# Performance work log

Measured on AMD Instinct MI355X. Metric: run time of the kernel, lower is better.

The kernel has to match this reference:

```python
import jax, jax.numpy as jnp
import numpy as np

C = 32          # d_model / channels
D_STATE = 32
D_CONV = 4
EXPAND = 2
D_INNER = EXPAND * C          # 64
DT_RANK = (C + 15) // 16      # ceil(32/16) = 2
EPS = 1e-5


def _conv2d(x, w, b):
    # x: (B,C,H,W), w: (O,I,3,3), stride 1, padding 1 (torch Conv2d)
    y = jax.lax.conv_general_dilated(
        x, w, window_strides=(1, 1), padding=[(1, 1), (1, 1)],
        dimension_numbers=("NCHW", "OIHW", "NCHW"))
    return y + b[None, :, None, None]


def _silu(x):
    return x * jax.nn.sigmoid(x)


def _mamba(xs, in_proj_w, conv1d_w, conv1d_b, x_proj_w, dt_proj_w, dt_proj_b,
           A_log, Dp, out_proj_w):
    # xs: (B, L, C)
    xz = xs @ in_proj_w.T                       # (B, L, 2*D_INNER)
    xm, z = jnp.split(xz, 2, axis=-1)           # each (B, L, D_INNER)

    # causal depthwise conv1d along L (torch: padding=d_conv-1 then [..., :L])
    xc = xm.transpose(0, 2, 1)                  # (B, D_INNER, L)
    xc = jax.lax.conv_general_dilated(
        xc, conv1d_w, window_strides=(1,), padding=[(D_CONV - 1, 0)],
        dimension_numbers=("NCH", "OIH", "NCH"),
        feature_group_count=D_INNER)
    xm = _silu((xc + conv1d_b[None, :, None]).transpose(0, 2, 1))  # (B,L,D_INNER)

    x_dbl = xm @ x_proj_w.T                     # (B, L, DT_RANK + 2*D_STATE)
    dt = x_dbl[..., :DT_RANK]
    Bm = x_dbl[..., DT_RANK:DT_RANK + D_STATE]  # (B, L, N)
    Cm = x_dbl[..., DT_RANK + D_STATE:]         # (B, L, N)

    delta = jax.nn.softplus(dt @ dt_proj_w.T + dt_proj_b)  # (B, L, D_INNER)
    A = -jnp.exp(A_log)                                     # (D_INNER, N)

    deltaA = jnp.exp(delta[..., None] * A)                           # (B,L,D,N)
    deltaBx = delta[..., None] * Bm[:, :, None, :] * xm[..., None]   # (B,L,D,N)

    def combine(c1, c2):
        a1, b1 = c1
        a2, b2 = c2
        return a1 * a2, a2 * b1 + b2

    # parallel linear recurrence h_t = deltaA_t * h_{t-1} + deltaBx_t
    _, hstate = jax.lax.associative_scan(combine, (deltaA, deltaBx), axis=1)

    y = jnp.einsum("bldn,bln->bld", hstate, Cm) + xm * Dp
    y = y * _silu(z)
    return y @ out_proj_w.T                     # (B, L, C)


def setup_inputs() -> dict:
    key = jax.random.key(0)
    ks = jax.random.split(key, 16)
    s = 0.02
    inp = {
        "x": jax.random.normal(ks[0], (4, C, 64, 64), dtype=jnp.float32),
        "conv1_w": jax.random.normal(ks[1], (2 * C, C, 3, 3), jnp.float32) * s,
        "conv1_b": jnp.zeros((2 * C,), jnp.float32),
        "conv2_w": jax.random.normal(ks[2], (C, 2 * C, 3, 3), jnp.float32) * s,
        "conv2_b": jnp.zeros((C,), jnp.float32),
        "ln_g": jnp.ones((C,), jnp.float32),
        "ln_b": jnp.zeros((C,), jnp.float32),
        "in_proj_w": jax.random.normal(ks[3], (2 * D_INNER, C), jnp.float32) * s,
        "conv1d_w": jax.random.normal(ks[4], (D_INNER, 1, D_CONV), jnp.float32) * 0.1,
        "conv1d_b": jnp.zeros((D_INNER,), jnp.float32),
        "x_proj_w": jax.random.normal(ks[5], (DT_RANK + 2 * D_STATE, D_INNER), jnp.float32) * s,
        "dt_proj_w": jax.random.normal(ks[6], (D_INNER, DT_RANK), jnp.float32) * 0.1,
        "dt_proj_b": jax.random.normal(ks[7], (D_INNER,), jnp.float32) * 0.1 - 4.0,
        "A_log": jnp.log(jnp.tile(jnp.arange(1, D_STATE + 1, dtype=jnp.float32), (D_INNER, 1))),
        "Dp": jnp.ones((D_INNER,), jnp.float32),
        "out_proj_w": jax.random.normal(ks[8], (C, D_INNER), jnp.float32) * s,
        "smooth_w": jax.random.normal(ks[9], (C, C, 3, 3), jnp.float32) * s,
        "smooth_b": jnp.zeros((C,), jnp.float32),
    }
    return inp


def reference(x, conv1_w, conv1_b, conv2_w, conv2_b, ln_g, ln_b,
              in_proj_w, conv1d_w, conv1d_b, x_proj_w, dt_proj_w, dt_proj_b,
              A_log, Dp, out_proj_w, smooth_w, smooth_b):
    b, c, h, w = x.shape
    # convb residual
    t = jax.nn.relu(_conv2d(x, conv1_w, conv1_b))
    x = _conv2d(t, conv2_w, conv2_b) + x
    # reshape (b,c,h,w) -> (b, h*w, c) row-major (faithful to torch .reshape)
    xs = x.reshape(b, -1, c)
    # LayerNorm over last dim
    mu = jnp.mean(xs, axis=-1, keepdims=True)
    var = jnp.mean(jnp.square(xs - mu), axis=-1, keepdims=True)
    xs = (xs - mu) * jax.lax.rsqrt(var + EPS) * ln_g + ln_b
    # Mamba block
    y = _mamba(xs, in_proj_w, conv1d_w, conv1d_b, x_proj_w, dt_proj_w,
               dt_proj_b, A_log, Dp, out_proj_w)
    y = y.transpose(0, 2, 1).reshape(b, c, h, w)
    return _conv2d(y, smooth_w, smooth_b)
```

## Files before the change

kernel.cpp:

```cpp
#include <hip/hip_runtime.h>
#include <math.h>

#define SEQL 4096
#define L2E 1.44269504088896340736f

#if defined(__has_builtin)
#if __has_builtin(__builtin_amdgcn_exp2f)
#define FAST_EXP2(x) __builtin_amdgcn_exp2f(x)
#endif
#endif
#ifndef FAST_EXP2
#define FAST_EXP2(x) exp2f(x)
#endif

__device__ __forceinline__ float sigmoid_f(float x){ return 1.0f/(1.0f+expf(-x)); }

template<int CI, int CO, int COG, bool RELU, bool RES>
__global__ __launch_bounds__(256) void conv3x3_k(const float* __restrict__ in,
    const float* __restrict__ wgt, const float* __restrict__ bias,
    const float* __restrict__ res, float* __restrict__ out)
{
  constexpr int CIT = CI/4;
  __shared__ float tin[4][2][6][72];
  __shared__ float red[3][4][COG][66];
  const int tid  = threadIdx.x;
  const int lane = tid & 63;
  const int ty   = tid >> 6;
  const int h0   = blockIdx.x * 4;
  const int co0  = blockIdx.y * COG;
  const int b    = blockIdx.z;

  if (lane < 24){
    int cl = lane / 12, rem = lane % 12, r = rem >> 1, side = rem & 1;
    tin[ty][cl][r][side ? 68 : 3] = 0.0f;
  }

  float acc[4][COG];
  #pragma unroll
  for (int rr=0;rr<4;++rr)
    #pragma unroll
    for (int u=0;u<COG;++u) acc[rr][u] = 0.0f;

  const int ci0 = ty*CIT;
  for (int cig = ci0; cig < ci0 + CIT; cig += 2){
    #pragma unroll
    for (int k=0;k<3;++k){
      int idx4 = lane + k*64;
      int row  = idx4 >> 4;
      int cl   = row / 6, r = row - cl*6;
      int w4   = (idx4 & 15) << 2;
      int h    = h0 - 1 + r;
      float4 v = make_float4(0.0f,0.0f,0.0f,0.0f);
      if (h >= 0 && h < 64)
        v = *(const float4*)(in + ((size_t)(b*CI+cig+cl)*64 + h)*64 + w4);
      *(float4*)&tin[ty][cl][r][4+w4] = v;
    }
    #pragma unroll
    for (int cl=0; cl<2; ++cl){
      float rv[6][3];
      #pragma unroll
      for (int r=0;r<6;++r)
        #pragma unroll
        for (int c=0;c<3;++c)
          rv[r][c] = tin[ty][cl][r][3+lane+c];
      #pragma unroll
      for (int u=0;u<COG;++u){
        const float* wp = wgt + ((size_t)(co0+u)*CI + cig + cl)*9;
        #pragma unroll
        for (int rr=0;rr<4;++rr)
          #pragma unroll
          for (int j=0;j<3;++j){
            acc[rr][u] = fmaf(rv[rr+j][0], wp[j*3+0], acc[rr][u]);
            acc[rr][u] = fmaf(rv[rr+j][1], wp[j*3+1], acc[rr][u]);
            acc[rr][u] = fmaf(rv[rr+j][2], wp[j*3+2], acc[rr][u]);
          }
      }
    }
  }
  if (ty > 0){
    #pragma unroll
    for (int rr=0;rr<4;++rr)
      #pragma unroll
      for (int u=0;u<COG;++u) red[ty-1][rr][u][lane] = acc[rr][u];
  }
  __syncthreads();
  if (ty == 0){
    #pragma unroll
    for (int rr=0;rr<4;++rr)
      #pragma unroll
      for (int u=0;u<COG;++u){
        float s = acc[rr][u] + red[0][rr][u][lane] + red[1][rr][u][lane]
                + red[2][rr][u][lane] + bias[co0+u];
        size_t ob = ((size_t)(b*CO+co0+u)*64 + h0+rr)*64 + lane;
        if constexpr (RES)  s += res[ob];
        if constexpr (RELU) s = fmaxf(s, 0.0f);
        out[ob] = s;
      }
  }
}

__global__ __launch_bounds__(512) void mamba_in_k(const float* __restrict__ x2,
    const float* __restrict__ g, const float* __restrict__ be,
    const float* __restrict__ Wip, const float* __restrict__ cw,
    const float* __restrict__ cb, const float* __restrict__ Wxp,
    const float* __restrict__ Wdt, const float* __restrict__ bdt,
    float* __restrict__ xm2, float* __restrict__ szb, float* __restrict__ dlt,
    float* __restrict__ Bm, float* __restrict__ Cm)
{
  __shared__ float xn[68][36];
  __shared__ float xm[64][68];
  __shared__ float xt[64][68];
  __shared__ float xd[64][68];
  const int tid = threadIdx.x, lane = tid & 63, ty = tid >> 6;
  const int bi = blockIdx.x >> 6;
  const int l0 = (blockIdx.x & 63) << 6;

  if (ty < 2){
    int t = ty*64 + lane;
    if (t < 67){
      int tok = l0 - 3 + t;
      if (tok >= 0){
        const float* row = x2 + (size_t)bi*131072 + (size_t)tok*32;
        float v[32];
        #pragma unroll
        for (int c=0;c<32;c+=4){
          float4 f = *(const float4*)(row + c);
          v[c]=f.x; v[c+1]=f.y; v[c+2]=f.z; v[c+3]=f.w;
        }
        float p[8];
        #pragma unroll
        for (int j2=0;j2<8;++j2) p[j2]=v[j2];
        #pragma unroll
        for (int i=8;i<32;i+=8){
          #pragma unroll
          for (int j2=0;j2<8;++j2) p[j2]+=v[i+j2];
        }
        float mu = (((p[0]+p[1])+(p[2]+p[3]))+((p[4]+p[5])+(p[6]+p[7]))) * 0.03125f;
        float q[8];
        #pragma unroll
        for (int j2=0;j2<8;++j2){ float dd=v[j2]-mu; q[j2]=dd*dd; }
        #pragma unroll
        for (int i=8;i<32;i+=8){
          #pragma unroll
          for (int j2=0;j2<8;++j2){ float dd=v[i+j2]-mu; q[j2]+=dd*dd; }
        }
        float var = (((q[0]+q[1])+(q[2]+q[3]))+((q[4]+q[5])+(q[6]+q[7]))) * 0.03125f;
        float rstd = 1.0f / sqrtf(var + 1e-5f);
        #pragma unroll
        for (int c=0;c<32;++c) xn[t][c] = (v[c]-mu)*rstd*g[c] + be[c];
      } else {
        #pragma unroll
        for (int c=0;c<32;++c) xn[t][c] = 0.0f;
      }
    }
  }
  __syncthreads();

  const int d0 = ty*8;
  {
    float xvA[32];
    #pragma unroll
    for (int c=0;c<32;c+=4){
      float4 f = *(const float4*)(&xn[lane][c]);
      xvA[c]=f.x; xvA[c+1]=f.y; xvA[c+2]=f.z; xvA[c+3]=f.w;
    }
    #pragma unroll
    for (int jj=0;jj<8;++jj){
      const float* wr = Wip + (d0+jj)*32;
      float a = 0.0f;
      #pragma unroll
      for (int c=0;c<32;++c) a = fmaf(xvA[c], wr[c], a);
      xm[d0+jj][lane] = a;
    }
  }
  if (lane < 3){
    float xvB[32];
    #pragma unroll
    for (int c=0;c<32;c+=4){
      float4 f = *(const float4*)(&xn[64+lane][c]);
      xvB[c]=f.x; xvB[c+1]=f.y; xvB[c+2]=f.z; xvB[c+3]=f.w;
    }
    #pragma unroll
    for (int jj=0;jj<8;++jj){
      const float* wr = Wip + (d0+jj)*32;
      float a = 0.0f;
      #pragma unroll
      for (int c=0;c<32;++c) a = fmaf(xvB[c], wr[c], a);
      xm[d0+jj][64+lane] = a;
    }
  }
  {
    float xvC[32];
    #pragma unroll
    for (int c=0;c<32;c+=4){
      float4 f = *(const float4*)(&xn[lane+3][c]);
      xvC[c]=f.x; xvC[c+1]=f.y; xvC[c+2]=f.z; xvC[c+3]=f.w;
    }
    #pragma unroll
    for (int jj=0;jj<8;++jj){
      const float* wr = Wip + (64+d0+jj)*32;
      float a = 0.0f;
      #pragma unroll
      for (int c=0;c<32;++c) a = fmaf(xvC[c], wr[c], a);
      szb[((size_t)(bi*64+d0+jj))*SEQL + l0 + lane] = a * sigmoid_f(a);
    }
  }
  __syncthreads();

  #pragma unroll
  for (int jj=0;jj<8;++jj){
    int d = d0 + jj;
    float a = xm[d][lane]*cw[d*4] + xm[d][lane+1]*cw[d*4+1]
            + xm[d][lane+2]*cw[d*4+2] + xm[d][lane+3]*cw[d*4+3] + cb[d];
    float s = a * sigmoid_f(a);
    xt[lane][d] = s;
    xm2[((size_t)(bi*64+d))*SEQL + l0 + lane] = s;
  }
  __syncthreads();

  float xv[64];
  #pragma unroll
  for (int c=0;c<64;c+=4){
    float4 f = *(const float4*)(&xt[lane][c]);
    xv[c]=f.x; xv[c+1]=f.y; xv[c+2]=f.z; xv[c+3]=f.w;
  }
  for (int j=ty; j<66; j+=8){
    const float* wr = Wxp + j*64;
    float a = 0.0f;
    #pragma unroll
    for (int c=0;c<64;++c) a = fmaf(xv[c], wr[c], a);
    xd[lane][j] = a;
  }
  __syncthreads();

  float dt0 = xd[lane][0], dt1 = xd[lane][1];
  #pragma unroll
  for (int k=0;k<8;++k){
    int d2 = ty*8 + k;
    float v = dt0*Wdt[d2*2] + dt1*Wdt[d2*2+1] + bdt[d2];
    float sp = fmaxf(v,0.0f) + log1pf(expf(-fabsf(v)));
    dlt[((size_t)(bi*64+d2))*SEQL + l0 + lane] = sp;
  }
  const int which = ty >> 2, gq = ty & 3;
  float* dst = which ? Cm : Bm;
  size_t base = ((size_t)bi*SEQL + l0 + lane)*32 + gq*8;
  const int s0 = 2 + which*32 + gq*8;
  float4 f0, f1;
  f0.x = xd[lane][s0+0]; f0.y = xd[lane][s0+1]; f0.z = xd[lane][s0+2]; f0.w = xd[lane][s0+3];
  f1.x = xd[lane][s0+4]; f1.y = xd[lane][s0+5]; f1.z = xd[lane][s0+6]; f1.w = xd[lane][s0+7];
  *(float4*)(dst + base)     = f0;
  *(float4*)(dst + base + 4) = f1;
}

__global__ __launch_bounds__(256) void scan_p1(const float* __restrict__ dlt,
    const float* __restrict__ xssm, const float* __restrict__ Bm,
    const float* __restrict__ A_log, float* __restrict__ cA, float* __restrict__ cH)
{
  const int tid = threadIdx.x;
  const int n = tid & 31;
  const int chunk = (blockIdx.x & 7)*8 + (tid >> 5);
  const int bd = blockIdx.x >> 3;
  const int b = bd >> 6, d = bd & 63;
  const int l0 = chunk << 6;
  const float Av2 = -expf(A_log[d*32+n]) * L2E;
  const float* del = dlt  + (size_t)bd*SEQL + l0;
  const float* xp  = xssm + (size_t)bd*SEQL + l0;
  const float* Bp  = Bm + ((size_t)b*SEQL + l0)*32 + n;
  float h = 0.0f, aP = 1.0f;
  #pragma unroll 4
  for (int i0=0;i0<64;i0+=4){
    float4 d4 = *(const float4*)(del+i0);
    float4 x4 = *(const float4*)(xp +i0);
    float b0 = Bp[(i0+0)*32], b1 = Bp[(i0+1)*32], b2 = Bp[(i0+2)*32], b3 = Bp[(i0+3)*32];
    float a0 = FAST_EXP2(d4.x*Av2); h = fmaf(a0,h, d4.x*b0*x4.x); aP *= a0;
    float a1 = FAST_EXP2(d4.y*Av2); h = fmaf(a1,h, d4.y*b1*x4.y); aP *= a1;
    float a2 = FAST_EXP2(d4.z*Av2); h = fmaf(a2,h, d4.z*b2*x4.z); aP *= a2;
    float a3 = FAST_EXP2(d4.w*Av2); h = fmaf(a3,h, d4.w*b3*x4.w); aP *= a3;
  }
  int idx = (bd*64+chunk)*32 + n;
  cA[idx] = aP; cH[idx] = h;
}

__global__ __launch_bounds__(128) void scan_comb(const float* __restrict__ cA,
    float* __restrict__ cH)
{
  const int gid = blockIdx.x*128 + threadIdx.x;
  const int n = gid & 31, bd = gid >> 5;
  const size_t base = (size_t)bd*64*32 + n;
  float hrun = 0.0f;
  #pragma unroll 8
  for (int c=0;c<64;++c){
    float ac = cA[base + c*32];
    float hc = cH[base + c*32];
    cH[base + c*32] = hrun;
    hrun = fmaf(ac, hrun, hc);
  }
}

__global__ __launch_bounds__(256) void scan_p2(const float* __restrict__ dlt,
    const float* __restrict__ xssm, const float* __restrict__ Bm,
    const float* __restrict__ Cm, const float* __restrict__ A_log,
    const float* __restrict__ Dp, const float* __restrict__ sz,
    const float* __restrict__ cH, float* __restrict__ yt)
{
  const int tid = threadIdx.x;
  const int n = tid & 31;
  const int chunk = (blockIdx.x & 7)*8 + (tid >> 5);
  const int bd = blockIdx.x >> 3;
  const int b = bd >> 6, d = bd & 63;
  const int l0 = chunk << 6;
  const float Av2 = -expf(A_log[d*32+n]) * L2E;
  const float Dv = Dp[d];
  const float* del = dlt  + (size_t)bd*SEQL + l0;
  const float* xp  = xssm + (size_t)bd*SEQL + l0;
  const float* szp = sz   + (size_t)bd*SEQL + l0;
  const float* Bp  = Bm + ((size_t)b*SEQL + l0)*32 + n;
  const float* Cp  = Cm + ((size_t)b*SEQL + l0)*32 + n;
  float* yp = yt + (size_t)bd*SEQL + l0;
  float h = cH[(bd*64+chunk)*32 + n];
  #pragma unroll 2
  for (int i0=0;i0<64;i0+=4){
    float4 d4 = *(const float4*)(del+i0);
    float4 x4 = *(const float4*)(xp +i0);
    float4 s4 = *(const float4*)(szp+i0);
    float b0 = Bp[(i0+0)*32], b1 = Bp[(i0+1)*32], b2 = Bp[(i0+2)*32], b3 = Bp[(i0+3)*32];
    float c0 = Cp[(i0+0)*32], c1 = Cp[(i0+1)*32], c2 = Cp[(i0+2)*32], c3 = Cp[(i0+3)*32];
    float a0 = FAST_EXP2(d4.x*Av2); h = fmaf(a0,h, d4.x*b0*x4.x);
    float v0 = h*c0;
    float a1 = FAST_EXP2(d4.y*Av2); h = fmaf(a1,h, d4.y*b1*x4.y);
    float v1 = h*c1;
    float a2 = FAST_EXP2(d4.z*Av2); h = fmaf(a2,h, d4.z*b2*x4.z);
    float v2 = h*c2;
    float a3 = FAST_EXP2(d4.w*Av2); h = fmaf(a3,h, d4.w*b3*x4.w);
    float v3 = h*c3;
    v0 += __shfl_xor(v0,16); v0 += __shfl_xor(v0,8); v0 += __shfl_xor(v0,4);
    v0 += __shfl_xor(v0,2);  v0 += __shfl_xor(v0,1);
    v1 += __shfl_xor(v1,16); v1 += __shfl_xor(v1,8); v1 += __shfl_xor(v1,4);
    v1 += __shfl_xor(v1,2);  v1 += __shfl_xor(v1,1);
    v2 += __shfl_xor(v2,16); v2 += __shfl_xor(v2,8); v2 += __shfl_xor(v2,4);
    v2 += __shfl_xor(v2,2);  v2 += __shfl_xor(v2,1);
    v3 += __shfl_xor(v3,16); v3 += __shfl_xor(v3,8); v3 += __shfl_xor(v3,4);
    v3 += __shfl_xor(v3,2);  v3 += __shfl_xor(v3,1);
    if (n==0){
      yp[i0+0] = fmaf(x4.x, Dv, v0) * s4.x;
      yp[i0+1] = fmaf(x4.y, Dv, v1) * s4.y;
      yp[i0+2] = fmaf(x4.z, Dv, v2) * s4.z;
      yp[i0+3] = fmaf(x4.w, Dv, v3) * s4.w;
    }
  }
}

__global__ __launch_bounds__(512) void outproj_k(const float* __restrict__ yt,
    const float* __restrict__ Wout, float* __restrict__ ym)
{
  __shared__ float ys[64][68];
  const int tid = threadIdx.x, lane = tid & 63, ty = tid >> 6;
  const int bi = blockIdx.x >> 6;
  const int l0 = (blockIdx.x & 63) << 6;
  for (int r=ty; r<64; r+=8)
    ys[lane][r] = yt[((size_t)(bi*64+r))*SEQL + l0 + lane];
  __syncthreads();
  float yv[64];
  #pragma unroll
  for (int c=0;c<64;c+=4){
    float4 f = *(const float4*)(&ys[lane][c]);
    yv[c]=f.x; yv[c+1]=f.y; yv[c+2]=f.z; yv[c+3]=f.w;
  }
  #pragma unroll
  for (int jj=0;jj<4;++jj){
    int j = ty*4 + jj;
    const float* wr = Wout + j*64;
    float acc = 0.0f;
    #pragma unroll
    for (int c=0;c<64;++c) acc = fmaf(yv[c], wr[c], acc);
    ym[((size_t)(bi*32+j))*SEQL + l0 + lane] = acc;
  }
}

extern "C" void kernel_launch(void* const* d_in, const int* in_sizes, int n_in,
                              void* d_out, int out_size, void* d_ws, size_t ws_size,
                              hipStream_t stream) {
  const float* x        = (const float*)d_in[0];
  const float* conv1_w  = (const float*)d_in[1];
  const float* conv1_b  = (const float*)d_in[2];
  const float* conv2_w  = (const float*)d_in[3];
  const float* conv2_b  = (const float*)d_in[4];
  const float* ln_g     = (const float*)d_in[5];
  const float* ln_b     = (const float*)d_in[6];
  const float* in_proj_w= (const float*)d_in[7];
  const float* conv1d_w = (const float*)d_in[8];
  const float* conv1d_b = (const float*)d_in[9];
  const float* x_proj_w = (const float*)d_in[10];
  const float* dt_proj_w= (const float*)d_in[11];
  const float* dt_proj_b= (const float*)d_in[12];
  const float* A_log    = (const float*)d_in[13];
  const float* Dp       = (const float*)d_in[14];
  const float* out_proj_w=(const float*)d_in[15];
  const float* smooth_w = (const float*)d_in[16];
  const float* smooth_b = (const float*)d_in[17];
  float* out = (float*)d_out;

  float* ws = (float*)d_ws;
  float* t      = ws;
  float* x2     = t      + 1048576;
  float* xm2    = x2     + 524288;
  float* szb    = xm2    + 1048576;
  float* dlt    = szb    + 1048576;
  float* Bmat   = dlt    + 1048576;
  float* Cmat   = Bmat   + 524288;
  float* yt     = Cmat   + 524288;
  float* ym     = yt     + 1048576;
  float* cA     = t;
  float* cH     = t + 524288;

  conv3x3_k<32,64,4,true ,false><<<dim3(16,16,4), 256, 0, stream>>>(x,  conv1_w, conv1_b, nullptr, t);
  conv3x3_k<64,32,4,false,true ><<<dim3(16,8,4), 256, 0, stream>>>(t,  conv2_w, conv2_b, x,       x2);
  mamba_in_k  <<<256, 512, 0, stream>>>(x2, ln_g, ln_b, in_proj_w, conv1d_w, conv1d_b,
                                        x_proj_w, dt_proj_w, dt_proj_b,
                                        xm2, szb, dlt, Bmat, Cmat);
  scan_p1     <<<2048, 256, 0, stream>>>(dlt, xm2, Bmat, A_log, cA, cH);
  scan_comb   <<<64,   128, 0, stream>>>(cA, cH);
  scan_p2     <<<2048, 256, 0, stream>>>(dlt, xm2, Bmat, Cmat, A_log, Dp, szb, cH, yt);
  outproj_k   <<<256, 512, 0, stream>>>(yt, out_proj_w, ym);
  conv3x3_k<32,32,4,false,false><<<dim3(16,8,4), 256, 0, stream>>>(ym, smooth_w, smooth_b, nullptr, out);
}
```

Measured before the change: 223.6 us.

## Pad shared tiles to odd strides and transpose chunk-state layout for vectorized scan

Shared-memory row strides in the Mamba input and out-projection kernels change from multiples of 4 to odd values (37, 67). Reads switch from float4 vector loads to scalar loads, which trades fewer LDS instructions for fewer bank conflicts. The chunk carry arrays cA/cH are re-laid out so each (bd,n) pair's 64 chunks are contiguous. This lets the inter-chunk combine kernel use float4 loads and stores instead of strided scalar accesses, at the cost of strided writes in the chunk-summary kernel and strided reads in scan_p2. The conv edits are cosmetic.

```diff
diff --git a/kernel.cpp b/kernel.cpp
--- a/kernel.cpp
+++ b/kernel.cpp
@@ -45,13 +45,13 @@
   for (int cig = ci0; cig < ci0 + CIT; cig += 2){
     #pragma unroll
     for (int k=0;k<3;++k){
-      int idx4 = lane + k*64;
+      int idx4 = lane + (k<<6);
       int row  = idx4 >> 4;
-      int cl   = row / 6, r = row - cl*6;
-      int w4   = (idx4 & 15) << 2;
-      int h    = h0 - 1 + r;
-      float4 v = make_float4(0.0f,0.0f,0.0f,0.0f);
-      if (h >= 0 && h < 64)
+      int cl = row/6, r = row - cl*6;
+      int w4 = (idx4 & 15) << 2;
+      int h  = h0 - 1 + r;
+      float4 v = make_float4(0.f,0.f,0.f,0.f);
+      if (h>=0 && h<64)
         v = *(const float4*)(in + ((size_t)(b*CI+cig+cl)*64 + h)*64 + w4);
       *(float4*)&tin[ty][cl][r][4+w4] = v;
     }
@@ -70,9 +70,9 @@
         for (int rr=0;rr<4;++rr)
           #pragma unroll
           for (int j=0;j<3;++j){
-            acc[rr][u] = fmaf(rv[rr+j][0], wp[j*3+0], acc[rr][u]);
-            acc[rr][u] = fmaf(rv[rr+j][1], wp[j*3+1], acc[rr][u]);
-            acc[rr][u] = fmaf(rv[rr+j][2], wp[j*3+2], acc[rr][u]);
+            acc[rr][u] = fmaf(rv[rr+j][0], wp[3*j+0], acc[rr][u]);
+            acc[rr][u] = fmaf(rv[rr+j][1], wp[3*j+1], acc[rr][u]);
+            acc[rr][u] = fmaf(rv[rr+j][2], wp[3*j+2], acc[rr][u]);
           }
       }
     }
@@ -107,10 +107,10 @@
     float* __restrict__ xm2, float* __restrict__ szb, float* __restrict__ dlt,
     float* __restrict__ Bm, float* __restrict__ Cm)
 {
-  __shared__ float xn[68][36];
+  __shared__ float xn[68][37];
   __shared__ float xm[64][68];
-  __shared__ float xt[64][68];
-  __shared__ float xd[64][68];
+  __shared__ float xt[64][67];
+  __shared__ float xd[64][67];
   const int tid = threadIdx.x, lane = tid & 63, ty = tid >> 6;
   const int bi = blockIdx.x >> 6;
   const int l0 = (blockIdx.x & 63) << 6;
@@ -160,10 +160,7 @@
   {
     float xvA[32];
     #pragma unroll
-    for (int c=0;c<32;c+=4){
-      float4 f = *(const float4*)(&xn[lane][c]);
-      xvA[c]=f.x; xvA[c+1]=f.y; xvA[c+2]=f.z; xvA[c+3]=f.w;
-    }
+    for (int c=0;c<32;++c) xvA[c] = xn[lane][c];
     #pragma unroll
     for (int jj=0;jj<8;++jj){
       const float* wr = Wip + (d0+jj)*32;
@@ -176,10 +173,7 @@
   if (lane < 3){
     float xvB[32];
     #pragma unroll
-    for (int c=0;c<32;c+=4){
-      float4 f = *(const float4*)(&xn[64+lane][c]);
-      xvB[c]=f.x; xvB[c+1]=f.y; xvB[c+2]=f.z; xvB[c+3]=f.w;
-    }
+    for (int c=0;c<32;++c) xvB[c] = xn[64+lane][c];
     #pragma unroll
     for (int jj=0;jj<8;++jj){
       const float* wr = Wip + (d0+jj)*32;
@@ -192,10 +186,7 @@
   {
     float xvC[32];
     #pragma unroll
-    for (int c=0;c<32;c+=4){
-      float4 f = *(const float4*)(&xn[lane+3][c]);
-      xvC[c]=f.x; xvC[c+1]=f.y; xvC[c+2]=f.z; xvC[c+3]=f.w;
-    }
+    for (int c=0;c<32;++c) xvC[c] = xn[lane+3][c];
     #pragma unroll
     for (int jj=0;jj<8;++jj){
       const float* wr = Wip + (64+d0+jj)*32;
@@ -220,10 +211,7 @@
 
   float xv[64];
   #pragma unroll
-  for (int c=0;c<64;c+=4){
-    float4 f = *(const float4*)(&xt[lane][c]);
-    xv[c]=f.x; xv[c+1]=f.y; xv[c+2]=f.z; xv[c+3]=f.w;
-  }
+  for (int c=0;c<64;++c) xv[c] = xt[lane][c];
   for (int j=ty; j<66; j+=8){
     const float* wr = Wxp + j*64;
     float a = 0.0f;
@@ -277,7 +265,7 @@
     float a2 = FAST_EXP2(d4.z*Av2); h = fmaf(a2,h, d4.z*b2*x4.z); aP *= a2;
     float a3 = FAST_EXP2(d4.w*Av2); h = fmaf(a3,h, d4.w*b3*x4.w); aP *= a3;
   }
-  int idx = (bd*64+chunk)*32 + n;
+  int idx = ((bd<<5) + n)*64 + chunk;
   cA[idx] = aP; cH[idx] = h;
 }
 
@@ -285,15 +273,18 @@
     float* __restrict__ cH)
 {
   const int gid = blockIdx.x*128 + threadIdx.x;
-  const int n = gid & 31, bd = gid >> 5;
-  const size_t base = (size_t)bd*64*32 + n;
+  const size_t base = (size_t)gid*64;
   float hrun = 0.0f;
-  #pragma unroll 8
-  for (int c=0;c<64;++c){
-    float ac = cA[base + c*32];
-    float hc = cH[base + c*32];
-    cH[base + c*32] = hrun;
-    hrun = fmaf(ac, hrun, hc);
+  #pragma unroll 4
+  for (int c0=0;c0<64;c0+=4){
+    float4 a4 = *(const float4*)(cA + base + c0);
+    float4 h4 = *(const float4*)(cH + base + c0);
+    float4 o;
+    o.x = hrun; hrun = fmaf(a4.x, hrun, h4.x);
+    o.y = hrun; hrun = fmaf(a4.y, hrun, h4.y);
+    o.z = hrun; hrun = fmaf(a4.z, hrun, h4.z);
+    o.w = hrun; hrun = fmaf(a4.w, hrun, h4.w);
+    *(float4*)(cH + base + c0) = o;
   }
 }
 
@@ -317,7 +308,7 @@
   const float* Bp  = Bm + ((size_t)b*SEQL + l0)*32 + n;
   const float* Cp  = Cm + ((size_t)b*SEQL + l0)*32 + n;
   float* yp = yt + (size_t)bd*SEQL + l0;
-  float h = cH[(bd*64+chunk)*32 + n];
+  float h = cH[((bd<<5) + n)*64 + chunk];
   #pragma unroll 2
   for (int i0=0;i0<64;i0+=4){
     float4 d4 = *(const float4*)(del+i0);
@@ -353,7 +344,7 @@
 __global__ __launch_bounds__(512) void outproj_k(const float* __restrict__ yt,
     const float* __restrict__ Wout, float* __restrict__ ym)
 {
-  __shared__ float ys[64][68];
+  __shared__ float ys[64][67];
   const int tid = threadIdx.x, lane = tid & 63, ty = tid >> 6;
   const int bi = blockIdx.x >> 6;
   const int l0 = (blockIdx.x & 63) << 6;
@@ -362,10 +353,7 @@
   __syncthreads();
   float yv[64];
   #pragma unroll
-  for (int c=0;c<64;c+=4){
-    float4 f = *(const float4*)(&ys[lane][c]);
-    yv[c]=f.x; yv[c+1]=f.y; yv[c+2]=f.z; yv[c+3]=f.w;
-  }
+  for (int c=0;c<64;++c) yv[c] = ys[lane][c];
   #pragma unroll
   for (int jj=0;jj<4;++jj){
     int j = ty*4 + jj;
```

Measured after the change: 227.8 us. About the same (+1.9%).
